# Optimization experiments

Measured on AMD Instinct MI355X. Metric: run time of the kernel, lower is better.

The kernel has to match this reference:

```python
import jax, jax.numpy as jnp
import numpy as np
from jax import lax

H = 512   # hidden_size
O = 256   # output_size
B = 64    # batch
S = 1024  # encoder sequence length
T = 256   # decoder timesteps


def setup_inputs() -> dict:
    key = jax.random.key(0)
    ks = jax.random.split(key, 10)
    bound = 1.0 / np.sqrt(H)  # PyTorch LSTM/Linear init scale
    return {
        "encoder_outputs": jax.random.normal(ks[0], (B, S, H), jnp.float32),
        "hidden": jax.random.normal(ks[1], (1, B, H), jnp.float32),
        "cell": jax.random.normal(ks[2], (1, B, H), jnp.float32),
        "target": jax.random.normal(ks[3], (B, T, O), jnp.float32),
        # LSTM params (gate order i, f, g, o as in PyTorch)
        "W_ih": jax.random.uniform(ks[4], (4 * H, H + O), jnp.float32, -bound, bound),
        "W_hh": jax.random.uniform(ks[5], (4 * H, H), jnp.float32, -bound, bound),
        "b_ih": jax.random.uniform(ks[6], (4 * H,), jnp.float32, -bound, bound),
        "b_hh": jax.random.uniform(ks[7], (4 * H,), jnp.float32, -bound, bound),
        # FC params
        "W_fc": jax.random.uniform(ks[8], (O, H), jnp.float32, -bound, bound),
        "b_fc": jax.random.uniform(ks[9], (O,), jnp.float32, -bound, bound),
    }


def reference(encoder_outputs, hidden, cell, target, W_ih, W_hh, b_ih, b_hh, W_fc, b_fc):
    h0 = hidden[0]  # [B, H]
    c0 = cell[0]    # [B, H]

    def step(carry, x_t):
        h, c = carry
        # Attention: dot-product scores over encoder positions
        scores = jnp.einsum("bsh,bh->bs", encoder_outputs, h)      # [B, S]
        attn = jax.nn.softmax(scores, axis=1)
        context = jnp.einsum("bs,bsh->bh", attn, encoder_outputs)  # [B, H]
        x = jnp.concatenate([context, x_t], axis=-1)               # [B, H+O]
        # Single-step LSTM cell (PyTorch gate order i, f, g, o)
        gates = x @ W_ih.T + b_ih + h @ W_hh.T + b_hh              # [B, 4H]
        i_g, f_g, g_g, o_g = jnp.split(gates, 4, axis=-1)
        i_g = jax.nn.sigmoid(i_g)
        f_g = jax.nn.sigmoid(f_g)
        g_g = jnp.tanh(g_g)
        o_g = jax.nn.sigmoid(o_g)
        c_new = f_g * c + i_g * g_g
        h_new = o_g * jnp.tanh(c_new)
        out = h_new @ W_fc.T + b_fc                                # [B, O]
        return (h_new, c_new), out

    _, outs = lax.scan(step, (h0, c0), jnp.swapaxes(target, 0, 1))  # outs: [T, B, O]
    return jnp.swapaxes(outs, 0, 1)  # [B, T, O]
```

## Files before the change

kernel.cpp:

```cpp
#include <hip/hip_runtime.h>

#define HH 512
#define OO 256
#define BB 64
#define SS 1024
#define TT 256
#define KK 1280

typedef __attribute__((ext_vector_type(8))) short bh8;
typedef __attribute__((ext_vector_type(8))) _Float16 hf8;
typedef __attribute__((ext_vector_type(4))) float fx4;
typedef unsigned short ushort_t;

__device__ __forceinline__ ushort_t f2bf(float x) {
    union { float f; unsigned int u; } v; v.f = x;
    unsigned int r = v.u + 0x7fffu + ((v.u >> 16) & 1u);
    return (ushort_t)(r >> 16);
}
__device__ __forceinline__ float bf2f(ushort_t s) {
    union { unsigned int u; float f; } z; z.u = ((unsigned int)s) << 16; return z.f;
}

__global__ void prep_weights(const float* __restrict__ W_ih,
                             const float* __restrict__ W_hh,
                             ushort_t* __restrict__ wfH,
                             ushort_t* __restrict__ wfL) {
    int g = blockIdx.x * 256 + threadIdx.x;
    if (g >= 64 * 40 * 2 * 64) return;
    int lane = g & 63;
    int nt = (g >> 6) & 1;
    int kk = (g >> 7) % 40;
    int ht = (g >> 7) / 40;
    int c = nt * 16 + (lane & 15);
    int gate = c >> 3, rr = c & 7;
    int j = gate * 512 + ht * 8 + rr;
    int kbase = kk * 32 + (lane >> 4) * 8;
    ushort_t* dh = wfH + (size_t)g * 8;
    ushort_t* dl = wfL + (size_t)g * 8;
#pragma unroll
    for (int r = 0; r < 8; ++r) {
        int k = kbase + r;
        float v = (k < 768) ? W_ih[(size_t)j * 768 + k]
                            : W_hh[(size_t)j * 512 + (k - 768)];
        ushort_t hi = f2bf(v);
        dh[r] = hi;
        dl[r] = f2bf(v - bf2f(hi));
    }
}

__global__ void prep_misc(const float* __restrict__ hidden,
                          const float* __restrict__ cell,
                          const float* __restrict__ W_fc,
                          float* __restrict__ h, float* __restrict__ c,
                          _Float16* __restrict__ wfc16) {
    const int total = 32768 + 32768 + 131072;
    for (int i = blockIdx.x * 256 + threadIdx.x; i < total; i += gridDim.x * 256) {
        if (i < 32768)       h[i] = hidden[i];
        else if (i < 65536)  c[i - 32768] = cell[i - 32768];
        else                 wfc16[i - 65536] = (_Float16)W_fc[i - 65536];
    }
}

__global__ void prep_ench(const float* __restrict__ enc,
                          _Float16* __restrict__ ench) {
    const size_t i = ((size_t)blockIdx.x * 256 + threadIdx.x) * 8;
    const float4 a = *(const float4*)(enc + i);
    const float4 b = *(const float4*)(enc + i + 4);
    hf8 o;
    o[0] = (_Float16)a.x; o[1] = (_Float16)a.y;
    o[2] = (_Float16)a.z; o[3] = (_Float16)a.w;
    o[4] = (_Float16)b.x; o[5] = (_Float16)b.y;
    o[6] = (_Float16)b.z; o[7] = (_Float16)b.w;
    *(hf8*)(ench + i) = o;
}

__device__ __forceinline__ void fc_unit(int v, int tprev,
                                        const float* __restrict__ h,
                                        const _Float16* __restrict__ wfc16,
                                        const float* __restrict__ b_fc,
                                        float* __restrict__ out,
                                        float (*shacc)[64]) {
    const int tid = threadIdx.x;
    const int b = v >> 2, oq = v & 3;
    const int ol = tid & 63, kq = tid >> 6;
    const int o = oq * 64 + ol;
    float acc = 0.f;
    const float* hp = h + b * HH + kq * 128;
    const _Float16* wp = wfc16 + (size_t)o * HH + kq * 128;
#pragma unroll 8
    for (int k2 = 0; k2 < 128; ++k2) acc += hp[k2] * (float)wp[k2];
    shacc[kq][ol] = acc;
    __syncthreads();
    if (tid < 64) {
        float vv = shacc[0][tid] + shacc[1][tid]
                 + shacc[2][tid] + shacc[3][tid] + b_fc[oq * 64 + tid];
        out[((size_t)b * TT + tprev) * OO + oq * 64 + tid] = vv;
    }
}

__global__ void __launch_bounds__(256)
step_attnp(int t, const _Float16* __restrict__ ench,
           const float* __restrict__ h,
           float* __restrict__ pm, float* __restrict__ pl,
           _Float16* __restrict__ pctx,
           const _Float16* __restrict__ wfc16, const float* __restrict__ b_fc,
           float* __restrict__ out) {
    const int tid = threadIdx.x;
    const int lane = tid & 63;
    const int w = tid >> 6;

    __shared__ union {
        struct { float m[4]; float l[4]; float ctx[4][512]; } a;
        struct { float acc[4][64]; } o;
    } sh;

    const int u = blockIdx.x;
    if (u < 1024) {
        const int b = u >> 4, ch = u & 15;
        float m = -3.0e38f, l = 0.f;
        const float* hb = h + b * HH + lane * 8;
        const float4 h0 = *(const float4*)hb;
        const float4 h1 = *(const float4*)(hb + 4);
        float cx[8];
#pragma unroll
        for (int j = 0; j < 8; ++j) cx[j] = 0.f;
        const _Float16* er =
            ench + ((size_t)(b * SS + ch * 64 + w * 16)) * HH + lane * 8;
        for (int g4 = 0; g4 < 4; ++g4) {
            const hf8 v0 = *(const hf8*)er;
            const hf8 v1 = *(const hf8*)(er + HH);
            const hf8 v2 = *(const hf8*)(er + 2 * HH);
            const hf8 v3 = *(const hf8*)(er + 3 * HH);
            float e0[8], e1[8], e2[8], e3[8];
#pragma unroll
            for (int j = 0; j < 8; ++j) {
                e0[j] = (float)v0[j]; e1[j] = (float)v1[j];
                e2[j] = (float)v2[j]; e3[j] = (float)v3[j];
            }
            float d0 = e0[0]*h0.x + e0[1]*h0.y + e0[2]*h0.z + e0[3]*h0.w
                     + e0[4]*h1.x + e0[5]*h1.y + e0[6]*h1.z + e0[7]*h1.w;
            float d1 = e1[0]*h0.x + e1[1]*h0.y + e1[2]*h0.z + e1[3]*h0.w
                     + e1[4]*h1.x + e1[5]*h1.y + e1[6]*h1.z + e1[7]*h1.w;
            float d2 = e2[0]*h0.x + e2[1]*h0.y + e2[2]*h0.z + e2[3]*h0.w
                     + e2[4]*h1.x + e2[5]*h1.y + e2[6]*h1.z + e2[7]*h1.w;
            float d3 = e3[0]*h0.x + e3[1]*h0.y + e3[2]*h0.z + e3[3]*h0.w
                     + e3[4]*h1.x + e3[5]*h1.y + e3[6]*h1.z + e3[7]*h1.w;
#pragma unroll
            for (int off = 32; off; off >>= 1) {
                d0 += __shfl_xor(d0, off);
                d1 += __shfl_xor(d1, off);
                d2 += __shfl_xor(d2, off);
                d3 += __shfl_xor(d3, off);
            }
            const float mx = fmaxf(fmaxf(d0, d1), fmaxf(d2, d3));
            if (mx > m) {
                const float fs = __expf(m - mx);
                l *= fs;
#pragma unroll
                for (int j = 0; j < 8; ++j) cx[j] *= fs;
                m = mx;
            }
            const float p0 = __expf(d0 - m);
            const float p1 = __expf(d1 - m);
            const float p2 = __expf(d2 - m);
            const float p3 = __expf(d3 - m);
            l += (p0 + p1) + (p2 + p3);
#pragma unroll
            for (int j = 0; j < 8; ++j)
                cx[j] += p0 * e0[j] + p1 * e1[j] + p2 * e2[j] + p3 * e3[j];
            er += 4 * HH;
        }
        if (lane == 0) { sh.a.m[w] = m; sh.a.l[w] = l; }
        *(float4*)&sh.a.ctx[w][lane * 8]     = make_float4(cx[0], cx[1], cx[2], cx[3]);
        *(float4*)&sh.a.ctx[w][lane * 8 + 4] = make_float4(cx[4], cx[5], cx[6], cx[7]);
        __syncthreads();
        float M = fmaxf(fmaxf(sh.a.m[0], sh.a.m[1]), fmaxf(sh.a.m[2], sh.a.m[3]));
        float wg[4]; float ls = 0.f;
#pragma unroll
        for (int q = 0; q < 4; ++q) { wg[q] = __expf(sh.a.m[q] - M); ls += wg[q] * sh.a.l[q]; }
        const int hh = tid * 2;
        float v0 = wg[0] * sh.a.ctx[0][hh] + wg[1] * sh.a.ctx[1][hh]
                 + wg[2] * sh.a.ctx[2][hh] + wg[3] * sh.a.ctx[3][hh];
        float v1 = wg[0] * sh.a.ctx[0][hh + 1] + wg[1] * sh.a.ctx[1][hh + 1]
                 + wg[2] * sh.a.ctx[2][hh + 1] + wg[3] * sh.a.ctx[3][hh + 1];
        _Float16* pc = pctx + ((size_t)(b * 16 + ch)) * HH;
        pc[hh]     = (_Float16)v0;
        pc[hh + 1] = (_Float16)v1;
        if (tid == 0) { pm[b * 16 + ch] = M; pl[b * 16 + ch] = ls; }
    } else if (t > 0) {
        fc_unit(u - 1024, t - 1, h, wfc16, b_fc, out, sh.o.acc);
    }
}

__global__ void __launch_bounds__(256)
step_combine(int t, const float* __restrict__ target, const float* __restrict__ h,
             const float* __restrict__ pm, const float* __restrict__ pl,
             const _Float16* __restrict__ pctx,
             ushort_t* __restrict__ xbh, ushort_t* __restrict__ xbl) {
    const int tid = threadIdx.x;
    const int b = blockIdx.x;
    float Mb = -3.0e38f;
#pragma unroll
    for (int q2 = 0; q2 < 16; ++q2) Mb = fmaxf(Mb, pm[b * 16 + q2]);
    float wq[16]; float lsb = 0.f;
#pragma unroll
    for (int q2 = 0; q2 < 16; ++q2) {
        wq[q2] = __expf(pm[b * 16 + q2] - Mb);
        lsb += wq[q2] * pl[b * 16 + q2];
    }
    const float inv = 1.0f / lsb;
    const int h2 = tid * 2;
    float s0 = 0.f, s1 = 0.f;
#pragma unroll
    for (int q2 = 0; q2 < 16; ++q2) {
        const _Float16* pc2 = pctx + ((size_t)(b * 16 + q2)) * HH + h2;
        s0 += wq[q2] * (float)pc2[0];
        s1 += wq[q2] * (float)pc2[1];
    }
    s0 *= inv; s1 *= inv;
    ushort_t a0 = f2bf(s0), a1 = f2bf(s1);
    xbh[b * KK + h2]     = a0;  xbl[b * KK + h2]     = f2bf(s0 - bf2f(a0));
    xbh[b * KK + h2 + 1] = a1;  xbl[b * KK + h2 + 1] = f2bf(s1 - bf2f(a1));
    if (tid < 128) {
        const float* tg = target + ((size_t)b * TT + t) * OO + tid * 2;
        ushort_t t0 = f2bf(tg[0]), t1 = f2bf(tg[1]);
        xbh[b * KK + 512 + tid * 2]     = t0;
        xbh[b * KK + 512 + tid * 2 + 1] = t1;
        xbl[b * KK + 512 + tid * 2]     = f2bf(tg[0] - bf2f(t0));
        xbl[b * KK + 512 + tid * 2 + 1] = f2bf(tg[1] - bf2f(t1));
    }
    const float hv0 = h[b * HH + h2], hv1 = h[b * HH + h2 + 1];
    ushort_t g0 = f2bf(hv0), g1 = f2bf(hv1);
    xbh[b * KK + 768 + h2]     = g0;  xbl[b * KK + 768 + h2]     = f2bf(hv0 - bf2f(g0));
    xbh[b * KK + 768 + h2 + 1] = g1;  xbl[b * KK + 768 + h2 + 1] = f2bf(hv1 - bf2f(g1));
}

__global__ void __launch_bounds__(256)
step_gates(const ushort_t* __restrict__ xbh,
           const ushort_t* __restrict__ xbl,
           const ushort_t* __restrict__ wfH,
           const ushort_t* __restrict__ wfL,
           const float* __restrict__ b_ih, const float* __restrict__ b_hh,
           float* __restrict__ h, float* __restrict__ c) {
    const int tid = threadIdx.x;
    const int lane = tid & 63;
    const int w = tid >> 6;
    __shared__ float g[64][32];

    const int ht = blockIdx.x;
    fx4 a0 = {0, 0, 0, 0}, a1 = {0, 0, 0, 0};
    const int bro = 16 * w + (lane & 15);
    const int kg = lane >> 4;
    const size_t wbase = (size_t)ht * 40 * 2 * 512;
    for (int kk = 0; kk < 40; ++kk) {
        const size_t aoff = (size_t)bro * KK + kk * 32 + kg * 8;
        bh8 avh = *(const bh8*)(xbh + aoff);
        bh8 avl = *(const bh8*)(xbl + aoff);
        bh8 b0h = *(const bh8*)(wfH + wbase + (kk * 2 + 0) * 512 + lane * 8);
        bh8 b1h = *(const bh8*)(wfH + wbase + (kk * 2 + 1) * 512 + lane * 8);
        bh8 b0l = *(const bh8*)(wfL + wbase + (kk * 2 + 0) * 512 + lane * 8);
        bh8 b1l = *(const bh8*)(wfL + wbase + (kk * 2 + 1) * 512 + lane * 8);
        a0 = __builtin_amdgcn_mfma_f32_16x16x32_bf16(avh, b0h, a0, 0, 0, 0);
        a0 = __builtin_amdgcn_mfma_f32_16x16x32_bf16(avl, b0h, a0, 0, 0, 0);
        a0 = __builtin_amdgcn_mfma_f32_16x16x32_bf16(avh, b0l, a0, 0, 0, 0);
        a1 = __builtin_amdgcn_mfma_f32_16x16x32_bf16(avh, b1h, a1, 0, 0, 0);
        a1 = __builtin_amdgcn_mfma_f32_16x16x32_bf16(avl, b1h, a1, 0, 0, 0);
        a1 = __builtin_amdgcn_mfma_f32_16x16x32_bf16(avh, b1l, a1, 0, 0, 0);
    }
    const int crow = (lane >> 4) * 4;
#pragma unroll
    for (int r = 0; r < 4; ++r) {
        g[16 * w + crow + r][lane & 15]        = a0[r];
        g[16 * w + crow + r][16 + (lane & 15)] = a1[r];
    }
    __syncthreads();
#pragma unroll
    for (int p = 0; p < 2; ++p) {
        const int idx = tid * 2 + p;
        const int b = idx >> 3, r = idx & 7;
        const int hidx = ht * 8 + r;
        float gi = g[b][r]      + b_ih[hidx]        + b_hh[hidx];
        float gf = g[b][8 + r]  + b_ih[512 + hidx]  + b_hh[512 + hidx];
        float gg = g[b][16 + r] + b_ih[1024 + hidx] + b_hh[1024 + hidx];
        float go = g[b][24 + r] + b_ih[1536 + hidx] + b_hh[1536 + hidx];
        float ig = 1.f / (1.f + __expf(-gi));
        float fg = 1.f / (1.f + __expf(-gf));
        float g2 = tanhf(gg);
        float og = 1.f / (1.f + __expf(-go));
        float cn = fg * c[b * HH + hidx] + ig * g2;
        float hn = og * tanhf(cn);
        c[b * HH + hidx] = cn;
        h[b * HH + hidx] = hn;
    }
}

__global__ void __launch_bounds__(256)
fc_final(const float* __restrict__ h, const _Float16* __restrict__ wfc16,
         const float* __restrict__ b_fc, float* __restrict__ out) {
    __shared__ float acc[4][64];
    fc_unit(blockIdx.x, TT - 1, h, wfc16, b_fc, out, acc);
}

extern "C" void kernel_launch(void* const* d_in, const int* in_sizes, int n_in,
                              void* d_out, int out_size, void* d_ws, size_t ws_size,
                              hipStream_t stream) {
    const float* enc    = (const float*)d_in[0];
    const float* hidden = (const float*)d_in[1];
    const float* cellp  = (const float*)d_in[2];
    const float* target = (const float*)d_in[3];
    const float* W_ih   = (const float*)d_in[4];
    const float* W_hh   = (const float*)d_in[5];
    const float* b_ih   = (const float*)d_in[6];
    const float* b_hh   = (const float*)d_in[7];
    const float* W_fc   = (const float*)d_in[8];
    const float* b_fc   = (const float*)d_in[9];
    float* out = (float*)d_out;

    char* base = (char*)d_ws;
    float* h            = (float*)(base + 0);
    float* c            = (float*)(base + 131072);
    ushort_t* wfH       = (ushort_t*)(base + 262144);
    ushort_t* wfL       = (ushort_t*)(base + 5505024);
    ushort_t* xbh       = (ushort_t*)(base + 10747904);
    ushort_t* xbl       = (ushort_t*)(base + 10911744);
    float* pm           = (float*)(base + 11075584);
    float* pl           = (float*)(base + 11079680);
    _Float16* wfc16     = (_Float16*)(base + 11083776);
    _Float16* pctx      = (_Float16*)(base + 11345920);
    _Float16* ench      = (_Float16*)(base + 12394496);

    prep_weights<<<dim3(1280), dim3(256), 0, stream>>>(W_ih, W_hh, wfH, wfL);
    prep_misc<<<dim3(768), dim3(256), 0, stream>>>(hidden, cellp, W_fc, h, c, wfc16);
    prep_ench<<<dim3(16384), dim3(256), 0, stream>>>(enc, ench);

    for (int t = 0; t < TT; ++t) {
        step_attnp<<<dim3(1280), dim3(256), 0, stream>>>(
            t, ench, h, pm, pl, pctx, wfc16, b_fc, out);
        step_combine<<<dim3(64), dim3(256), 0, stream>>>(
            t, target, h, pm, pl, pctx, xbh, xbl);
        step_gates<<<dim3(64), dim3(256), 0, stream>>>(
            xbh, xbl, wfH, wfL, b_ih, b_hh, h, c);
    }
    fc_final<<<dim3(256), dim3(256), 0, stream>>>(h, wfc16, b_fc, out);
}
```

Baseline: 10.65 ms.

## Use packed fp16 dot2 in attention and split combine/gates across more blocks

The attention kernel now computes scores and context accumulation with packed fp16 dot2 instructions instead of converting encoder values to fp32 and doing scalar FMAs. The hidden state and the softmax probabilities are rounded to fp16 before the dot products, which lowers precision. The combine and gates kernels are split over 128 blocks instead of 64. Each gates block now handles half the batch rows with one N-tile per wave, which raises parallelism on the serial per-step kernels.

```diff
diff --git a/kernel.cpp b/kernel.cpp
--- a/kernel.cpp
+++ b/kernel.cpp
@@ -9,6 +9,7 @@
 
 typedef __attribute__((ext_vector_type(8))) short bh8;
 typedef __attribute__((ext_vector_type(8))) _Float16 hf8;
+typedef __attribute__((ext_vector_type(2))) _Float16 h2;
 typedef __attribute__((ext_vector_type(4))) float fx4;
 typedef unsigned short ushort_t;
 
@@ -119,8 +120,10 @@
         const int b = u >> 4, ch = u & 15;
         float m = -3.0e38f, l = 0.f;
         const float* hb = h + b * HH + lane * 8;
-        const float4 h0 = *(const float4*)hb;
-        const float4 h1 = *(const float4*)(hb + 4);
+        h2 hp[4];
+#pragma unroll
+        for (int i = 0; i < 4; ++i)
+            hp[i] = (h2){(_Float16)hb[2 * i], (_Float16)hb[2 * i + 1]};
         float cx[8];
 #pragma unroll
         for (int j = 0; j < 8; ++j) cx[j] = 0.f;
@@ -131,20 +134,18 @@
             const hf8 v1 = *(const hf8*)(er + HH);
             const hf8 v2 = *(const hf8*)(er + 2 * HH);
             const hf8 v3 = *(const hf8*)(er + 3 * HH);
-            float e0[8], e1[8], e2[8], e3[8];
-#pragma unroll
-            for (int j = 0; j < 8; ++j) {
-                e0[j] = (float)v0[j]; e1[j] = (float)v1[j];
-                e2[j] = (float)v2[j]; e3[j] = (float)v3[j];
+            const h2* q0 = (const h2*)&v0;
+            const h2* q1 = (const h2*)&v1;
+            const h2* q2 = (const h2*)&v2;
+            const h2* q3 = (const h2*)&v3;
+            float d0 = 0.f, d1 = 0.f, d2 = 0.f, d3 = 0.f;
+#pragma unroll
+            for (int i = 0; i < 4; ++i) {
+                d0 = __builtin_amdgcn_fdot2(q0[i], hp[i], d0, false);
+                d1 = __builtin_amdgcn_fdot2(q1[i], hp[i], d1, false);
+                d2 = __builtin_amdgcn_fdot2(q2[i], hp[i], d2, false);
+                d3 = __builtin_amdgcn_fdot2(q3[i], hp[i], d3, false);
             }
-            float d0 = e0[0]*h0.x + e0[1]*h0.y + e0[2]*h0.z + e0[3]*h0.w
-                     + e0[4]*h1.x + e0[5]*h1.y + e0[6]*h1.z + e0[7]*h1.w;
-            float d1 = e1[0]*h0.x + e1[1]*h0.y + e1[2]*h0.z + e1[3]*h0.w
-                     + e1[4]*h1.x + e1[5]*h1.y + e1[6]*h1.z + e1[7]*h1.w;
-            float d2 = e2[0]*h0.x + e2[1]*h0.y + e2[2]*h0.z + e2[3]*h0.w
-                     + e2[4]*h1.x + e2[5]*h1.y + e2[6]*h1.z + e2[7]*h1.w;
-            float d3 = e3[0]*h0.x + e3[1]*h0.y + e3[2]*h0.z + e3[3]*h0.w
-                     + e3[4]*h1.x + e3[5]*h1.y + e3[6]*h1.z + e3[7]*h1.w;
 #pragma unroll
             for (int off = 32; off; off >>= 1) {
                 d0 += __shfl_xor(d0, off);
@@ -165,9 +166,13 @@
             const float p2 = __expf(d2 - m);
             const float p3 = __expf(d3 - m);
             l += (p0 + p1) + (p2 + p3);
-#pragma unroll
-            for (int j = 0; j < 8; ++j)
-                cx[j] += p0 * e0[j] + p1 * e1[j] + p2 * e2[j] + p3 * e3[j];
+            const h2 pk01 = (h2){(_Float16)p0, (_Float16)p1};
+            const h2 pk23 = (h2){(_Float16)p2, (_Float16)p3};
+#pragma unroll
+            for (int j = 0; j < 8; ++j) {
+                cx[j] = __builtin_amdgcn_fdot2((h2){v0[j], v1[j]}, pk01, cx[j], false);
+                cx[j] = __builtin_amdgcn_fdot2((h2){v2[j], v3[j]}, pk23, cx[j], false);
+            }
             er += 4 * HH;
         }
         if (lane == 0) { sh.a.m[w] = m; sh.a.l[w] = l; }
@@ -198,7 +203,7 @@
              const _Float16* __restrict__ pctx,
              ushort_t* __restrict__ xbh, ushort_t* __restrict__ xbl) {
     const int tid = threadIdx.x;
-    const int b = blockIdx.x;
+    const int b = blockIdx.x >> 1, hf = blockIdx.x & 1;
     float Mb = -3.0e38f;
 #pragma unroll
     for (int q2 = 0; q2 < 16; ++q2) Mb = fmaxf(Mb, pm[b * 16 + q2]);
@@ -209,30 +214,29 @@
         lsb += wq[q2] * pl[b * 16 + q2];
     }
     const float inv = 1.0f / lsb;
-    const int h2 = tid * 2;
-    float s0 = 0.f, s1 = 0.f;
-#pragma unroll
-    for (int q2 = 0; q2 < 16; ++q2) {
-        const _Float16* pc2 = pctx + ((size_t)(b * 16 + q2)) * HH + h2;
-        s0 += wq[q2] * (float)pc2[0];
-        s1 += wq[q2] * (float)pc2[1];
-    }
-    s0 *= inv; s1 *= inv;
-    ushort_t a0 = f2bf(s0), a1 = f2bf(s1);
-    xbh[b * KK + h2]     = a0;  xbl[b * KK + h2]     = f2bf(s0 - bf2f(a0));
-    xbh[b * KK + h2 + 1] = a1;  xbl[b * KK + h2 + 1] = f2bf(s1 - bf2f(a1));
-    if (tid < 128) {
-        const float* tg = target + ((size_t)b * TT + t) * OO + tid * 2;
-        ushort_t t0 = f2bf(tg[0]), t1 = f2bf(tg[1]);
-        xbh[b * KK + 512 + tid * 2]     = t0;
-        xbh[b * KK + 512 + tid * 2 + 1] = t1;
-        xbl[b * KK + 512 + tid * 2]     = f2bf(tg[0] - bf2f(t0));
-        xbl[b * KK + 512 + tid * 2 + 1] = f2bf(tg[1] - bf2f(t1));
-    }
-    const float hv0 = h[b * HH + h2], hv1 = h[b * HH + h2 + 1];
-    ushort_t g0 = f2bf(hv0), g1 = f2bf(hv1);
-    xbh[b * KK + 768 + h2]     = g0;  xbl[b * KK + 768 + h2]     = f2bf(hv0 - bf2f(g0));
-    xbh[b * KK + 768 + h2 + 1] = g1;  xbl[b * KK + 768 + h2 + 1] = f2bf(hv1 - bf2f(g1));
+    const int col = hf * 256 + tid;
+    float s = 0.f;
+#pragma unroll
+    for (int q2 = 0; q2 < 16; ++q2)
+        s += wq[q2] * (float)pctx[((size_t)(b * 16 + q2)) * HH + col];
+    s *= inv;
+    const ushort_t a0 = f2bf(s);
+    xbh[b * KK + col] = a0;
+    xbl[b * KK + col] = f2bf(s - bf2f(a0));
+    if (hf == 0) {
+        const float tv = target[((size_t)b * TT + t) * OO + tid];
+        const ushort_t t0 = f2bf(tv);
+        xbh[b * KK + 512 + tid] = t0;
+        xbl[b * KK + 512 + tid] = f2bf(tv - bf2f(t0));
+    } else {
+        const int h2i = tid * 2;
+        const float hv0 = h[b * HH + h2i], hv1 = h[b * HH + h2i + 1];
+        const ushort_t g0 = f2bf(hv0), g1 = f2bf(hv1);
+        xbh[b * KK + 768 + h2i]     = g0;
+        xbl[b * KK + 768 + h2i]     = f2bf(hv0 - bf2f(g0));
+        xbh[b * KK + 768 + h2i + 1] = g1;
+        xbl[b * KK + 768 + h2i + 1] = f2bf(hv1 - bf2f(g1));
+    }
 }
 
 __global__ void __launch_bounds__(256)
@@ -245,44 +249,38 @@
     const int tid = threadIdx.x;
     const int lane = tid & 63;
     const int w = tid >> 6;
-    __shared__ float g[64][32];
-
-    const int ht = blockIdx.x;
-    fx4 a0 = {0, 0, 0, 0}, a1 = {0, 0, 0, 0};
-    const int bro = 16 * w + (lane & 15);
+    __shared__ float g[32][32];
+
+    const int bh = blockIdx.x >> 6;
+    const int ht = blockIdx.x & 63;
+    const int nt = w >> 1;
+    fx4 a0 = {0, 0, 0, 0};
+    const int bro = bh * 32 + 16 * (w & 1) + (lane & 15);
     const int kg = lane >> 4;
     const size_t wbase = (size_t)ht * 40 * 2 * 512;
     for (int kk = 0; kk < 40; ++kk) {
         const size_t aoff = (size_t)bro * KK + kk * 32 + kg * 8;
         bh8 avh = *(const bh8*)(xbh + aoff);
         bh8 avl = *(const bh8*)(xbl + aoff);
-        bh8 b0h = *(const bh8*)(wfH + wbase + (kk * 2 + 0) * 512 + lane * 8);
-        bh8 b1h = *(const bh8*)(wfH + wbase + (kk * 2 + 1) * 512 + lane * 8);
-        bh8 b0l = *(const bh8*)(wfL + wbase + (kk * 2 + 0) * 512 + lane * 8);
-        bh8 b1l = *(const bh8*)(wfL + wbase + (kk * 2 + 1) * 512 + lane * 8);
-        a0 = __builtin_amdgcn_mfma_f32_16x16x32_bf16(avh, b0h, a0, 0, 0, 0);
-        a0 = __builtin_amdgcn_mfma_f32_16x16x32_bf16(avl, b0h, a0, 0, 0, 0);
-        a0 = __builtin_amdgcn_mfma_f32_16x16x32_bf16(avh, b0l, a0, 0, 0, 0);
-        a1 = __builtin_amdgcn_mfma_f32_16x16x32_bf16(avh, b1h, a1, 0, 0, 0);
-        a1 = __builtin_amdgcn_mfma_f32_16x16x32_bf16(avl, b1h, a1, 0, 0, 0);
-        a1 = __builtin_amdgcn_mfma_f32_16x16x32_bf16(avh, b1l, a1, 0, 0, 0);
+        bh8 bhv = *(const bh8*)(wfH + wbase + (kk * 2 + nt) * 512 + lane * 8);
+        bh8 blv = *(const bh8*)(wfL + wbase + (kk * 2 + nt) * 512 + lane * 8);
+        a0 = __builtin_amdgcn_mfma_f32_16x16x32_bf16(avh, bhv, a0, 0, 0, 0);
+        a0 = __builtin_amdgcn_mfma_f32_16x16x32_bf16(avl, bhv, a0, 0, 0, 0);
+        a0 = __builtin_amdgcn_mfma_f32_16x16x32_bf16(avh, blv, a0, 0, 0, 0);
     }
     const int crow = (lane >> 4) * 4;
 #pragma unroll
-    for (int r = 0; r < 4; ++r) {
-        g[16 * w + crow + r][lane & 15]        = a0[r];
-        g[16 * w + crow + r][16 + (lane & 15)] = a1[r];
-    }
+    for (int r = 0; r < 4; ++r)
+        g[16 * (w & 1) + crow + r][nt * 16 + (lane & 15)] = a0[r];
     __syncthreads();
-#pragma unroll
-    for (int p = 0; p < 2; ++p) {
-        const int idx = tid * 2 + p;
-        const int b = idx >> 3, r = idx & 7;
+    {
+        const int lb = tid >> 3, r = tid & 7;
+        const int b = bh * 32 + lb;
         const int hidx = ht * 8 + r;
-        float gi = g[b][r]      + b_ih[hidx]        + b_hh[hidx];
-        float gf = g[b][8 + r]  + b_ih[512 + hidx]  + b_hh[512 + hidx];
-        float gg = g[b][16 + r] + b_ih[1024 + hidx] + b_hh[1024 + hidx];
-        float go = g[b][24 + r] + b_ih[1536 + hidx] + b_hh[1536 + hidx];
+        float gi = g[lb][r]      + b_ih[hidx]        + b_hh[hidx];
+        float gf = g[lb][8 + r]  + b_ih[512 + hidx]  + b_hh[512 + hidx];
+        float gg = g[lb][16 + r] + b_ih[1024 + hidx] + b_hh[1024 + hidx];
+        float go = g[lb][24 + r] + b_ih[1536 + hidx] + b_hh[1536 + hidx];
         float ig = 1.f / (1.f + __expf(-gi));
         float fg = 1.f / (1.f + __expf(-gf));
         float g2 = tanhf(gg);
@@ -336,9 +334,9 @@
     for (int t = 0; t < TT; ++t) {
         step_attnp<<<dim3(1280), dim3(256), 0, stream>>>(
             t, ench, h, pm, pl, pctx, wfc16, b_fc, out);
-        step_combine<<<dim3(64), dim3(256), 0, stream>>>(
+        step_combine<<<dim3(128), dim3(256), 0, stream>>>(
             t, target, h, pm, pl, pctx, xbh, xbl);
-        step_gates<<<dim3(64), dim3(256), 0, stream>>>(
+        step_gates<<<dim3(128), dim3(256), 0, stream>>>(
             xbh, xbl, wfH, wfL, b_ih, b_hh, h, c);
     }
     fc_final<<<dim3(256), dim3(256), 0, stream>>>(h, wfc16, b_fc, out);
```

Result: faster. 8.680 ms (median of 2 runs) (-18.5%).
